# Performance work log

Measured on AMD Instinct MI355X. Metric: run time of the kernel, lower is better.

Reference implementation:

```python
import jax, jax.numpy as jnp
import numpy as np

B, T, VOCAB_SZ, N_SPK = 64, 1024, 34, 128
D_TXT, D_SPK, H, N_MELS = 512, 64, 256, 80


def _lstm_params(key, in_dim, hid):
    k1, k2, k3, k4 = jax.random.split(key, 4)
    s = 1.0 / np.sqrt(hid)
    Wih = jax.random.uniform(k1, (4 * hid, in_dim), jnp.float32, -s, s)
    Whh = jax.random.uniform(k2, (4 * hid, hid), jnp.float32, -s, s)
    bih = jax.random.uniform(k3, (4 * hid,), jnp.float32, -s, s)
    bhh = jax.random.uniform(k4, (4 * hid,), jnp.float32, -s, s)
    return Wih, Whh, bih, bhh


def setup_inputs() -> dict:
    key = jax.random.key(0)
    ks = jax.random.split(key, 10)
    text_seq = jax.random.randint(ks[0], (B, T), 0, VOCAB_SZ)
    mel_spectrogram = jax.random.normal(ks[1], (B, T, N_MELS), jnp.float32)
    speaker_id = jax.random.randint(ks[2], (B,), 0, N_SPK)
    emb_text = jax.random.normal(ks[3], (VOCAB_SZ, D_TXT), jnp.float32)
    emb_text = emb_text.at[0].set(0.0)  # padding_idx=0
    emb_spk = jax.random.normal(ks[4], (N_SPK, D_SPK), jnp.float32)
    Wih_f, Whh_f, bih_f, bhh_f = _lstm_params(ks[5], D_TXT + D_SPK, H)
    Wih_b, Whh_b, bih_b, bhh_b = _lstm_params(ks[6], D_TXT + D_SPK, H)
    Wih_d, _Whh_d, bih_d, bhh_d = _lstm_params(ks[7], N_MELS + 2 * H, H)
    s = 1.0 / np.sqrt(H)
    Wfc = jax.random.uniform(ks[8], (N_MELS, H), jnp.float32, -s, s)
    bfc = jax.random.uniform(ks[9], (N_MELS,), jnp.float32, -s, s)
    return dict(text_seq=text_seq, mel_spectrogram=mel_spectrogram, speaker_id=speaker_id,
                emb_text=emb_text, emb_spk=emb_spk,
                Wih_f=Wih_f, Whh_f=Whh_f, bih_f=bih_f, bhh_f=bhh_f,
                Wih_b=Wih_b, Whh_b=Whh_b, bih_b=bih_b, bhh_b=bhh_b,
                Wih_d=Wih_d, bih_d=bih_d, bhh_d=bhh_d, Wfc=Wfc, bfc=bfc)


def _lstm_scan(xs, Wih, Whh, bih, bhh, reverse=False):
    # xs: [T, B, D] -> hs: [T, B, H] (PyTorch gate order i,f,g,o)
    nB, hid = xs.shape[1], Whh.shape[1]
    bias = bih + bhh
    def step(carry, x):
        h, c = carry
        g = x @ Wih.T + h @ Whh.T + bias
        i, f, gg, o = jnp.split(g, 4, axis=-1)
        c = jax.nn.sigmoid(f) * c + jax.nn.sigmoid(i) * jnp.tanh(gg)
        h = jax.nn.sigmoid(o) * jnp.tanh(c)
        return (h, c), h
    init = (jnp.zeros((nB, hid), xs.dtype), jnp.zeros((nB, hid), xs.dtype))
    _, hs = jax.lax.scan(step, init, xs, reverse=reverse)
    return hs


def reference(text_seq, mel_spectrogram, speaker_id, emb_text, emb_spk,
              Wih_f, Whh_f, bih_f, bhh_f, Wih_b, Whh_b, bih_b, bhh_b,
              Wih_d, bih_d, bhh_d, Wfc, bfc):
    text_embed = emb_text[text_seq]                       # [B, T, 512]
    spk = jnp.broadcast_to(emb_spk[speaker_id][:, None, :],
                           (text_seq.shape[0], text_seq.shape[1], emb_spk.shape[1]))
    enc_in = jnp.concatenate([text_embed, spk], axis=-1)  # [B, T, 576]
    xs = jnp.transpose(enc_in, (1, 0, 2))                 # time-major [T, B, 576]
    h_fwd = _lstm_scan(xs, Wih_f, Whh_f, bih_f, bhh_f)
    h_bwd = _lstm_scan(xs, Wih_b, Whh_b, bih_b, bhh_b, reverse=True)
    enc_out = jnp.concatenate([h_fwd, h_bwd], axis=-1)    # [T, B, 512]

    max_len = min(mel_spectrogram.shape[1], enc_out.shape[0])
    # Decoder: hidden state is reset (None) every step in the original, so
    # c = sigmoid(i)*tanh(g), h = sigmoid(o)*tanh(c); Whh contributes nothing.
    dbias = bih_d + bhh_d
    def dstep(prev_mel, e_t):
        x = jnp.concatenate([prev_mel, e_t], axis=-1)     # [B, 592]
        g = x @ Wih_d.T + dbias
        i, f, gg, o = jnp.split(g, 4, axis=-1)
        c = jax.nn.sigmoid(i) * jnp.tanh(gg)
        h = jax.nn.sigmoid(o) * jnp.tanh(c)
        out = h @ Wfc.T + bfc
        return out, out
    _, outs = jax.lax.scan(dstep, mel_spectrogram[:, 0, :], enc_out[: max_len - 1])
    return jnp.transpose(outs, (1, 0, 2))                 # [B, max_len-1, 80]
```

## Files before the change

kernel.cpp:

```cpp
#include <hip/hip_runtime.h>
#include <hip/hip_fp16.h>
#include <stdint.h>

#define T_SEQ 1024
#define NB    64
#define VOCAB 34
#define NSPK  128
#define DTXT  512
#define HID   256
#define NMEL  80
#define GROWS 1024
#define DROWS 768

typedef _Float16 f16;
typedef _Float16 f16x2 __attribute__((ext_vector_type(2)));
typedef _Float16 v8h __attribute__((ext_vector_type(8)));
typedef float v4f __attribute__((ext_vector_type(4)));

__device__ __forceinline__ float fdot2f(uint32_t a, uint32_t b, float c) {
  return __builtin_amdgcn_fdot2(__builtin_bit_cast(f16x2, a),
                                __builtin_bit_cast(f16x2, b), c, false);
}
__device__ __forceinline__ float sigm(float x) { return 1.0f / (1.0f + __expf(-x)); }
__device__ __forceinline__ float tanhf_fast(float x) {
  float e = __expf(2.0f * x);
  return 1.0f - 2.0f / (e + 1.0f);
}


__global__ void k_tp(const float* __restrict__ Wf, const float* __restrict__ Wb,
                     const float* __restrict__ emb_text, float* __restrict__ TP) {
  int blk = blockIdx.x; int dir = blk / VOCAB; int v = blk - dir * VOCAB;
  const float* W = dir ? Wb : Wf;
  const float* e = emb_text + (size_t)v * DTXT;
  for (int r = threadIdx.x; r < GROWS; r += 256) {
    const float* wr = W + (size_t)r * 576;
    float a0 = 0, a1 = 0, a2 = 0, a3 = 0;
    for (int d = 0; d < DTXT; d += 4) {
      a0 += e[d] * wr[d];     a1 += e[d+1] * wr[d+1];
      a2 += e[d+2] * wr[d+2]; a3 += e[d+3] * wr[d+3];
    }
    TP[(size_t)(dir * VOCAB + v) * GROWS + r] = (a0 + a1) + (a2 + a3);
  }
}

__global__ void k_sp(const float* __restrict__ Wf, const float* __restrict__ Wb,
                     const float* __restrict__ bihf, const float* __restrict__ bhhf,
                     const float* __restrict__ bihb, const float* __restrict__ bhhb,
                     const float* __restrict__ emb_spk, float* __restrict__ SP) {
  int blk = blockIdx.x; int dir = blk >> 7; int s = blk & 127;
  const float* W  = dir ? Wb : Wf;
  const float* bi = dir ? bihb : bihf;
  const float* bh = dir ? bhhb : bhhf;
  const float* e  = emb_spk + (size_t)s * 64;
  for (int r = threadIdx.x; r < GROWS; r += 256) {
    const float* wr = W + (size_t)r * 576 + 512;
    float acc = bi[r] + bh[r];
    for (int d = 0; d < 64; ++d) acc += e[d] * wr[d];
    SP[(size_t)(dir * NSPK + s) * GROWS + r] = acc;
  }
}

__global__ void k_whh(const float* __restrict__ Whhf, const float* __restrict__ Whhb,
                      f16* __restrict__ WhhH) {
  int idx = blockIdx.x * 256 + threadIdx.x;
  if (idx < 2 * GROWS * HID) {
    int dir = idx >> 18; int rem = idx & (GROWS * HID - 1);
    WhhH[idx] = (f16)(dir ? Whhb[rem] : Whhf[rem]);
  }
}

__global__ void k_decw(const float* __restrict__ Wih_d, const float* __restrict__ bih_d,
                       const float* __restrict__ bhh_d,
                       f16* __restrict__ WmH, f16* __restrict__ WdH, float* __restrict__ dbias) {
  int r = blockIdx.x;
  int src = (r < 256) ? r : (r + 256);
  const float* w = Wih_d + (size_t)src * 592;
  for (int k = threadIdx.x; k < 592; k += 256) {
    float v = w[k];
    if (k < 80) WmH[(size_t)r * 80 + k] = (f16)v;
    else        WdH[(size_t)r * 512 + (k - 80)] = (f16)v;
  }
  if (threadIdx.x == 0) dbias[r] = bih_d[src] + bhh_d[src];
}

__global__ void k_misc(const float* __restrict__ Wfc, f16* __restrict__ WfcH) {
  int idx = blockIdx.x * 256 + threadIdx.x;
  if (idx < NMEL * HID) WfcH[idx] = (f16)Wfc[idx];
}

__launch_bounds__(512, 2)
__global__ void k_enc(const int* __restrict__ text_seq, const int* __restrict__ speaker_id,
                      const float* __restrict__ TP, const float* __restrict__ SP,
                      const uint32_t* __restrict__ WhhH_dw,
                      f16* __restrict__ Hh) {
  __shared__ __align__(16) uint4 wtail[8 * 512];
  __shared__ __align__(16) uint32_t hbuf[2][128];
  __shared__ float pp[4][256];
  __shared__ int tseq[T_SEQ];

  int wg = blockIdx.x;
  int dir = wg >> 6, b = wg & 63;
  int tid = threadIdx.x;
  int u = tid & 255, kh = tid >> 8;

  uint4 w0[14], w1[14], w2[14], w3[14];
  {
    const uint4* p0 = (const uint4*)(WhhH_dw + ((size_t)(dir << 10) + u      ) * 128 + (kh << 6));
    const uint4* p1 = (const uint4*)(WhhH_dw + ((size_t)(dir << 10) + u + 256) * 128 + (kh << 6));
    const uint4* p2 = (const uint4*)(WhhH_dw + ((size_t)(dir << 10) + u + 512) * 128 + (kh << 6));
    const uint4* p3 = (const uint4*)(WhhH_dw + ((size_t)(dir << 10) + u + 768) * 128 + (kh << 6));
    #pragma unroll
    for (int i = 0; i < 14; ++i) { w0[i] = p0[i]; w1[i] = p1[i]; w2[i] = p2[i]; w3[i] = p3[i]; }
    #pragma unroll
    for (int j = 0; j < 2; ++j) {
      wtail[(0 * 2 + j) * 512 + tid] = p0[14 + j];
      wtail[(1 * 2 + j) * 512 + tid] = p1[14 + j];
      wtail[(2 * 2 + j) * 512 + tid] = p2[14 + j];
      wtail[(3 * 2 + j) * 512 + tid] = p3[14 + j];
    }
  }
  for (int i = tid; i < T_SEQ; i += 512) tseq[i] = text_seq[b * T_SEQ + i];
  if (tid < 128) hbuf[0][tid] = 0u;
  float sp0 = 0, sp1 = 0, sp2 = 0, sp3 = 0;
  if (kh == 0) {
    int spk = speaker_id[b];
    sp0 = SP[(size_t)(dir * NSPK + spk) * GROWS + u];
    sp1 = SP[(size_t)(dir * NSPK + spk) * GROWS + u + 256];
    sp2 = SP[(size_t)(dir * NSPK + spk) * GROWS + u + 512];
    sp3 = SP[(size_t)(dir * NSPK + spk) * GROWS + u + 768];
  }
  const float* TPd = TP + (size_t)dir * VOCAB * GROWS;
  float c_state = 0.0f;
  __syncthreads();

  float x0 = 0, x1 = 0, x2 = 0, x3 = 0;
  if (kh == 0) {
    int v = tseq[dir ? (T_SEQ - 1) : 0];
    x0 = TPd[(size_t)v * GROWS + u];
    x1 = TPd[(size_t)v * GROWS + u + 256];
    x2 = TPd[(size_t)v * GROWS + u + 512];
    x3 = TPd[(size_t)v * GROWS + u + 768];
  }

  float h_keep = 0.0f; int t_keep = 0;
  for (int n = 0; n < T_SEQ; ++n) {
    int t = dir ? (T_SEQ - 1 - n) : n;
    float xn0 = 0, xn1 = 0, xn2 = 0, xn3 = 0;
    if (kh == 0) {
      if (n > 0)
        Hh[((size_t)(dir * T_SEQ + t_keep) * NB + b) * HID + u] = (f16)h_keep;
      int tn = dir ? (T_SEQ - 2 - n) : (n + 1);
      tn = tn < 0 ? 0 : (tn > T_SEQ - 1 ? T_SEQ - 1 : tn);
      int vn = tseq[tn];
      xn0 = TPd[(size_t)vn * GROWS + u];
      xn1 = TPd[(size_t)vn * GROWS + u + 256];
      xn2 = TPd[(size_t)vn * GROWS + u + 512];
      xn3 = TPd[(size_t)vn * GROWS + u + 768];
    }

    float i0 = 0, i1 = 0, f0 = 0, f1 = 0, g0 = 0, g1 = 0, o0 = 0, o1 = 0;
    const uint4* h4 = ((const uint4*)hbuf[n & 1]) + (kh << 4);
    #pragma unroll
    for (int c = 0; c < 14; ++c) {
      uint4 hv = h4[c];
      i0 = fdot2f(w0[c].x, hv.x, i0); f0 = fdot2f(w1[c].x, hv.x, f0);
      g0 = fdot2f(w2[c].x, hv.x, g0); o0 = fdot2f(w3[c].x, hv.x, o0);
      i1 = fdot2f(w0[c].y, hv.y, i1); f1 = fdot2f(w1[c].y, hv.y, f1);
      g1 = fdot2f(w2[c].y, hv.y, g1); o1 = fdot2f(w3[c].y, hv.y, o1);
      i0 = fdot2f(w0[c].z, hv.z, i0); f0 = fdot2f(w1[c].z, hv.z, f0);
      g0 = fdot2f(w2[c].z, hv.z, g0); o0 = fdot2f(w3[c].z, hv.z, o0);
      i1 = fdot2f(w0[c].w, hv.w, i1); f1 = fdot2f(w1[c].w, hv.w, f1);
      g1 = fdot2f(w2[c].w, hv.w, g1); o1 = fdot2f(w3[c].w, hv.w, o1);
    }
    #pragma unroll
    for (int j = 0; j < 2; ++j) {
      uint4 hv = h4[14 + j];
      uint4 t0v = wtail[(0 * 2 + j) * 512 + tid];
      uint4 t1v = wtail[(1 * 2 + j) * 512 + tid];
      uint4 t2v = wtail[(2 * 2 + j) * 512 + tid];
      uint4 t3v = wtail[(3 * 2 + j) * 512 + tid];
      i0 = fdot2f(t0v.x, hv.x, i0); f0 = fdot2f(t1v.x, hv.x, f0);
      g0 = fdot2f(t2v.x, hv.x, g0); o0 = fdot2f(t3v.x, hv.x, o0);
      i1 = fdot2f(t0v.y, hv.y, i1); f1 = fdot2f(t1v.y, hv.y, f1);
      g1 = fdot2f(t2v.y, hv.y, g1); o1 = fdot2f(t3v.y, hv.y, o1);
      i0 = fdot2f(t0v.z, hv.z, i0); f0 = fdot2f(t1v.z, hv.z, f0);
      g0 = fdot2f(t2v.z, hv.z, g0); o0 = fdot2f(t3v.z, hv.z, o0);
      i1 = fdot2f(t0v.w, hv.w, i1); f1 = fdot2f(t1v.w, hv.w, f1);
      g1 = fdot2f(t2v.w, hv.w, g1); o1 = fdot2f(t3v.w, hv.w, o1);
    }
    if (kh == 1) {
      pp[0][u] = i0 + i1;
      pp[1][u] = f0 + f1;
      pp[2][u] = g0 + g1;
      pp[3][u] = o0 + o1;
    }
    __syncthreads();

    if (kh == 0) {
      float gi = (i0 + i1) + pp[0][u] + x0 + sp0;
      float gf = (f0 + f1) + pp[1][u] + x1 + sp1;
      float gg = (g0 + g1) + pp[2][u] + x2 + sp2;
      float go = (o0 + o1) + pp[3][u] + x3 + sp3;
      c_state = sigm(gf) * c_state + sigm(gi) * tanhf_fast(gg);
      float h = sigm(go) * tanhf_fast(c_state);
      ((f16*)hbuf[(n + 1) & 1])[u] = (f16)h;
      h_keep = h; t_keep = t;
      x0 = xn0; x1 = xn1; x2 = xn2; x3 = xn3;
    }
    __syncthreads();
  }
  if (kh == 0)
    Hh[((size_t)(dir * T_SEQ + t_keep) * NB + b) * HID + u] = (f16)h_keep;
}

__launch_bounds__(256, 4)
__global__ void k_eproj(const uint32_t* __restrict__ Hdw, const uint32_t* __restrict__ WdH_dw,
                        const float* __restrict__ dbias, f16* __restrict__ E) {
  __shared__ __align__(16) uint32_t Asm[64][68];
  __shared__ __align__(16) uint32_t Wsm[64][68];
  int nt = blockIdx.x % 12;
  int t  = blockIdx.x / 12;
  int n0 = nt * 64;
  int tid = threadIdx.x;
  int wave = tid >> 6, lane = tid & 63;
  int lr = lane & 15, lg = lane >> 4;

  v4f acc0 = {0,0,0,0}, acc1 = {0,0,0,0}, acc2 = {0,0,0,0}, acc3 = {0,0,0,0};

  for (int ch = 0; ch < 4; ++ch) {
    int dirc = ch >> 1, koff = (ch & 1) * 64;
    {
      int bb = tid >> 2, p = tid & 3;
      const uint32_t* asrc = Hdw + ((size_t)(dirc * T_SEQ + t) * NB + bb) * 128 + koff + p * 4;
      const uint32_t* wsrc = WdH_dw + (size_t)(n0 + bb) * 256 + ch * 64 + p * 4;
      #pragma unroll
      for (int q = 0; q < 4; ++q) {
        *(uint4*)(&Asm[bb][p * 4 + q * 16]) = *(const uint4*)(asrc + q * 16);
        *(uint4*)(&Wsm[bb][p * 4 + q * 16]) = *(const uint4*)(wsrc + q * 16);
      }
    }
    __syncthreads();
    #pragma unroll
    for (int sub = 0; sub < 4; ++sub) {
      v8h af = __builtin_bit_cast(v8h, *(const uint4*)&Asm[wave * 16 + lr][sub * 16 + lg * 4]);
      v8h b0 = __builtin_bit_cast(v8h, *(const uint4*)&Wsm[ 0 + lr][sub * 16 + lg * 4]);
      v8h b1 = __builtin_bit_cast(v8h, *(const uint4*)&Wsm[16 + lr][sub * 16 + lg * 4]);
      v8h b2 = __builtin_bit_cast(v8h, *(const uint4*)&Wsm[32 + lr][sub * 16 + lg * 4]);
      v8h b3 = __builtin_bit_cast(v8h, *(const uint4*)&Wsm[48 + lr][sub * 16 + lg * 4]);
      acc0 = __builtin_amdgcn_mfma_f32_16x16x32_f16(af, b0, acc0, 0, 0, 0);
      acc1 = __builtin_amdgcn_mfma_f32_16x16x32_f16(af, b1, acc1, 0, 0, 0);
      acc2 = __builtin_amdgcn_mfma_f32_16x16x32_f16(af, b2, acc2, 0, 0, 0);
      acc3 = __builtin_amdgcn_mfma_f32_16x16x32_f16(af, b3, acc3, 0, 0, 0);
    }
    __syncthreads();
  }

  float db0 = dbias[n0 +  0 + lr];
  float db1 = dbias[n0 + 16 + lr];
  float db2 = dbias[n0 + 32 + lr];
  float db3 = dbias[n0 + 48 + lr];
  #pragma unroll
  for (int reg = 0; reg < 4; ++reg) {
    int m = wave * 16 + lg * 4 + reg;
    f16* Erow = E + ((size_t)t * NB + m) * DROWS + n0;
    Erow[ 0 + lr] = (f16)(acc0[reg] + db0);
    Erow[16 + lr] = (f16)(acc1[reg] + db1);
    Erow[32 + lr] = (f16)(acc2[reg] + db2);
    Erow[48 + lr] = (f16)(acc3[reg] + db3);
  }
}

__launch_bounds__(512, 2)
__global__ void k_dec(const float* __restrict__ mel, const f16* __restrict__ E,
                      const uint32_t* __restrict__ WmH_dw, const uint32_t* __restrict__ WfcH_dw,
                      const float* __restrict__ bfc, float* __restrict__ out) {
  __shared__ __align__(16) uint32_t pm[40];
  __shared__ __align__(16) uint32_t h_sm[128];
  __shared__ float pp[3][256];
  __shared__ float partial[80][4];
  __shared__ __align__(16) uint4 Ebuf[2][16 * 96];

  int b = blockIdx.x;
  int tid = threadIdx.x;
  int u = tid & 255, kh = tid >> 8;

  uint4 wm0[5], wm1[5], wm2[5];
  {
    const uint4* p0 = (const uint4*)(WmH_dw + (size_t)(u      ) * 40) + kh * 5;
    const uint4* p1 = (const uint4*)(WmH_dw + (size_t)(u + 256) * 40) + kh * 5;
    const uint4* p2 = (const uint4*)(WmH_dw + (size_t)(u + 512) * 40) + kh * 5;
    #pragma unroll
    for (int k = 0; k < 5; ++k) { wm0[k] = p0[k]; wm1[k] = p1[k]; wm2[k] = p2[k]; }
  }
  int fr = (tid < 320) ? (tid >> 2) : 0;
  int q  = tid & 3;
  uint4 wfc[8];
  {
    const uint4* wp = (const uint4*)(WfcH_dw + (size_t)fr * 128) + q * 8;
    #pragma unroll
    for (int k = 0; k < 8; ++k) wfc[k] = wp[k];
  }
  float bfcv = bfc[tid < NMEL ? tid : 0];
  if (tid < 40) {
    float m0 = mel[(size_t)b * T_SEQ * NMEL + 2 * tid];
    float m1 = mel[(size_t)b * T_SEQ * NMEL + 2 * tid + 1];
    f16x2 v; v[0] = (f16)m0; v[1] = (f16)m1;
    pm[tid] = __builtin_bit_cast(uint32_t, v);
  }

  int srow = tid >> 5, scol = tid & 31;
  {
    const uint4* src = (const uint4*)(E + ((size_t)srow * NB + b) * DROWS);
    Ebuf[0][srow * 96 + scol     ] = src[scol];
    Ebuf[0][srow * 96 + scol + 32] = src[scol + 32];
    Ebuf[0][srow * 96 + scol + 64] = src[scol + 64];
  }
  __syncthreads();

  float o_keep = 0.0f;
  for (int t = 0; t < T_SEQ - 1; ++t) {
    int w = t >> 4, s = t & 15;
    if (t > 0 && tid < NMEL)
      out[((size_t)b * (T_SEQ - 1) + (t - 1)) * NMEL + tid] = o_keep;
    uint4 st0, st1, st2;
    bool do_stage = (s == 0) && (w < 63);
    if (do_stage) {
      int rr = (w + 1) * 16 + srow; if (rr > T_SEQ - 2) rr = T_SEQ - 2;
      const uint4* src = (const uint4*)(E + ((size_t)rr * NB + b) * DROWS);
      st0 = src[scol]; st1 = src[scol + 32]; st2 = src[scol + 64];
    }

    float a0 = 0, a1 = 0, a2 = 0;
    const uint4* pm4 = ((const uint4*)pm) + kh * 5;
    #pragma unroll
    for (int k = 0; k < 5; ++k) {
      uint4 hp = pm4[k];
      a0 = fdot2f(wm0[k].x, hp.x, a0); a1 = fdot2f(wm1[k].x, hp.x, a1); a2 = fdot2f(wm2[k].x, hp.x, a2);
      a0 = fdot2f(wm0[k].y, hp.y, a0); a1 = fdot2f(wm1[k].y, hp.y, a1); a2 = fdot2f(wm2[k].y, hp.y, a2);
      a0 = fdot2f(wm0[k].z, hp.z, a0); a1 = fdot2f(wm1[k].z, hp.z, a1); a2 = fdot2f(wm2[k].z, hp.z, a2);
      a0 = fdot2f(wm0[k].w, hp.w, a0); a1 = fdot2f(wm1[k].w, hp.w, a1); a2 = fdot2f(wm2[k].w, hp.w, a2);
    }
    if (kh == 1) { pp[0][u] = a0; pp[1][u] = a1; pp[2][u] = a2; }
    __syncthreads();

    if (kh == 0) {
      const f16* Erow = (const f16*)&Ebuf[w & 1][s * 96];
      float gi = a0 + pp[0][u] + (float)Erow[u];
      float gg = a1 + pp[1][u] + (float)Erow[u + 256];
      float go = a2 + pp[2][u] + (float)Erow[u + 512];
      float cc = sigm(gi) * tanhf_fast(gg);
      float h  = sigm(go) * tanhf_fast(cc);
      ((f16*)h_sm)[u] = (f16)h;
    }
    if (do_stage) {
      Ebuf[(w + 1) & 1][srow * 96 + scol     ] = st0;
      Ebuf[(w + 1) & 1][srow * 96 + scol + 32] = st1;
      Ebuf[(w + 1) & 1][srow * 96 + scol + 64] = st2;
    }
    __syncthreads();

    if (tid < 320) {
      const uint4* hrow = ((const uint4*)h_sm) + q * 8;
      float s0 = 0, s1 = 0, s2 = 0, s3 = 0;
      #pragma unroll
      for (int kk = 0; kk < 8; ++kk) {
        uint4 hq = hrow[kk];
        s0 = fdot2f(wfc[kk].x, hq.x, s0); s1 = fdot2f(wfc[kk].y, hq.y, s1);
        s2 = fdot2f(wfc[kk].z, hq.z, s2); s3 = fdot2f(wfc[kk].w, hq.w, s3);
      }
      partial[fr][q] = (s0 + s1) + (s2 + s3);
    }
    __syncthreads();

    if (tid < NMEL) {
      float o = ((partial[tid][0] + partial[tid][1]) +
                 (partial[tid][2] + partial[tid][3])) + bfcv;
      o_keep = o;
      ((f16*)pm)[tid] = (f16)o;
    }
    __syncthreads();
  }
  if (tid < NMEL)
    out[((size_t)b * (T_SEQ - 1) + (T_SEQ - 2)) * NMEL + tid] = o_keep;
}

extern "C" void kernel_launch(void* const* d_in, const int* in_sizes, int n_in,
                              void* d_out, int out_size, void* d_ws, size_t ws_size,
                              hipStream_t stream) {
  const int*   text_seq   = (const int*)d_in[0];
  const float* mel        = (const float*)d_in[1];
  const int*   speaker_id = (const int*)d_in[2];
  const float* emb_text   = (const float*)d_in[3];
  const float* emb_spk    = (const float*)d_in[4];
  const float* Wih_f = (const float*)d_in[5];
  const float* Whh_f = (const float*)d_in[6];
  const float* bih_f = (const float*)d_in[7];
  const float* bhh_f = (const float*)d_in[8];
  const float* Wih_b = (const float*)d_in[9];
  const float* Whh_b = (const float*)d_in[10];
  const float* bih_b = (const float*)d_in[11];
  const float* bhh_b = (const float*)d_in[12];
  const float* Wih_d = (const float*)d_in[13];
  const float* bih_d = (const float*)d_in[14];
  const float* bhh_d = (const float*)d_in[15];
  const float* Wfc   = (const float*)d_in[16];
  const float* bfc   = (const float*)d_in[17];
  float* out = (float*)d_out;

  char* base = (char*)d_ws;
  size_t off = 0;
  auto take = [&](size_t n) -> char* {
    off = (off + 255) & ~(size_t)255;
    char* r = base + off;
    off += n;
    return r;
  };
  float*        TP    = (float*)take((size_t)2 * VOCAB * GROWS * 4);
  float*        SP    = (float*)take((size_t)2 * NSPK * GROWS * 4);
  f16*          WhhH  = (f16*)take((size_t)2 * GROWS * HID * 2);
  f16*          WmH   = (f16*)take((size_t)DROWS * 80 * 2);
  f16*          WdH   = (f16*)take((size_t)DROWS * 512 * 2);
  f16*          WfcH  = (f16*)take((size_t)NMEL * HID * 2);
  float*        dbias = (float*)take((size_t)DROWS * 4);
  f16*          Hh    = (f16*)take((size_t)2 * T_SEQ * NB * HID * 2);
  f16*          E     = (f16*)take((size_t)(T_SEQ - 1) * NB * DROWS * 2);
  if (off > ws_size) return;

  k_tp  <<<2 * VOCAB, 256, 0, stream>>>(Wih_f, Wih_b, emb_text, TP);
  k_sp  <<<2 * NSPK, 256, 0, stream>>>(Wih_f, Wih_b, bih_f, bhh_f, bih_b, bhh_b, emb_spk, SP);
  k_whh <<<2048, 256, 0, stream>>>(Whh_f, Whh_b, WhhH);
  k_decw<<<DROWS, 256, 0, stream>>>(Wih_d, bih_d, bhh_d, WmH, WdH, dbias);
  k_misc<<<80, 256, 0, stream>>>(Wfc, WfcH);
  k_enc <<<128, 512, 0, stream>>>(text_seq, speaker_id, TP, SP,
                                  (const uint32_t*)WhhH, Hh);
  k_eproj<<<(T_SEQ - 1) * 12, 256, 0, stream>>>((const uint32_t*)Hh,
                                                (const uint32_t*)WdH, dbias, E);
  k_dec <<<NB, 512, 0, stream>>>(mel, E, (const uint32_t*)WmH,
                                 (const uint32_t*)WfcH, bfc, out);
}
```

Measured before the change: 3.023 ms.

## Pair adjacent lanes for K-split and reduce via shuffles instead of LDS barriers

Remaps the encoder and decoder threads so the two K-halves of each hidden unit sit in adjacent lanes and combines them with a lane shuffle, removing the LDS partial-sum buffers and one block barrier per time step. The decoder's FC reduction likewise uses shuffles across four adjacent lanes, which drops another barrier per step. Both lanes of a pair now compute the gate nonlinearities redundantly, and the encoder moves more of its Whh weights from registers to LDS (12 register chunks instead of 14), which adds LDS traffic in every step.

```diff
diff --git a/kernel.cpp b/kernel.cpp
--- a/kernel.cpp
+++ b/kernel.cpp
@@ -94,48 +94,44 @@
                       const float* __restrict__ TP, const float* __restrict__ SP,
                       const uint32_t* __restrict__ WhhH_dw,
                       f16* __restrict__ Hh) {
-  __shared__ __align__(16) uint4 wtail[8 * 512];
+  __shared__ __align__(16) uint4 wtail[16 * 512];
   __shared__ __align__(16) uint32_t hbuf[2][128];
-  __shared__ float pp[4][256];
   __shared__ int tseq[T_SEQ];
 
   int wg = blockIdx.x;
   int dir = wg >> 6, b = wg & 63;
   int tid = threadIdx.x;
-  int u = tid & 255, kh = tid >> 8;
-
-  uint4 w0[14], w1[14], w2[14], w3[14];
+  int u = tid >> 1, kh = tid & 1;
+
+  uint4 w0[12], w1[12], w2[12], w3[12];
   {
     const uint4* p0 = (const uint4*)(WhhH_dw + ((size_t)(dir << 10) + u      ) * 128 + (kh << 6));
     const uint4* p1 = (const uint4*)(WhhH_dw + ((size_t)(dir << 10) + u + 256) * 128 + (kh << 6));
     const uint4* p2 = (const uint4*)(WhhH_dw + ((size_t)(dir << 10) + u + 512) * 128 + (kh << 6));
     const uint4* p3 = (const uint4*)(WhhH_dw + ((size_t)(dir << 10) + u + 768) * 128 + (kh << 6));
     #pragma unroll
-    for (int i = 0; i < 14; ++i) { w0[i] = p0[i]; w1[i] = p1[i]; w2[i] = p2[i]; w3[i] = p3[i]; }
-    #pragma unroll
-    for (int j = 0; j < 2; ++j) {
-      wtail[(0 * 2 + j) * 512 + tid] = p0[14 + j];
-      wtail[(1 * 2 + j) * 512 + tid] = p1[14 + j];
-      wtail[(2 * 2 + j) * 512 + tid] = p2[14 + j];
-      wtail[(3 * 2 + j) * 512 + tid] = p3[14 + j];
+    for (int i = 0; i < 12; ++i) { w0[i] = p0[i]; w1[i] = p1[i]; w2[i] = p2[i]; w3[i] = p3[i]; }
+    #pragma unroll
+    for (int j = 0; j < 4; ++j) {
+      wtail[(0 * 4 + j) * 512 + tid] = p0[12 + j];
+      wtail[(1 * 4 + j) * 512 + tid] = p1[12 + j];
+      wtail[(2 * 4 + j) * 512 + tid] = p2[12 + j];
+      wtail[(3 * 4 + j) * 512 + tid] = p3[12 + j];
     }
   }
   for (int i = tid; i < T_SEQ; i += 512) tseq[i] = text_seq[b * T_SEQ + i];
   if (tid < 128) hbuf[0][tid] = 0u;
-  float sp0 = 0, sp1 = 0, sp2 = 0, sp3 = 0;
-  if (kh == 0) {
-    int spk = speaker_id[b];
-    sp0 = SP[(size_t)(dir * NSPK + spk) * GROWS + u];
-    sp1 = SP[(size_t)(dir * NSPK + spk) * GROWS + u + 256];
-    sp2 = SP[(size_t)(dir * NSPK + spk) * GROWS + u + 512];
-    sp3 = SP[(size_t)(dir * NSPK + spk) * GROWS + u + 768];
-  }
+  int spk = speaker_id[b];
+  float sp0 = SP[(size_t)(dir * NSPK + spk) * GROWS + u];
+  float sp1 = SP[(size_t)(dir * NSPK + spk) * GROWS + u + 256];
+  float sp2 = SP[(size_t)(dir * NSPK + spk) * GROWS + u + 512];
+  float sp3 = SP[(size_t)(dir * NSPK + spk) * GROWS + u + 768];
   const float* TPd = TP + (size_t)dir * VOCAB * GROWS;
   float c_state = 0.0f;
   __syncthreads();
 
-  float x0 = 0, x1 = 0, x2 = 0, x3 = 0;
-  if (kh == 0) {
+  float x0, x1, x2, x3;
+  {
     int v = tseq[dir ? (T_SEQ - 1) : 0];
     x0 = TPd[(size_t)v * GROWS + u];
     x1 = TPd[(size_t)v * GROWS + u + 256];
@@ -146,23 +142,20 @@
   float h_keep = 0.0f; int t_keep = 0;
   for (int n = 0; n < T_SEQ; ++n) {
     int t = dir ? (T_SEQ - 1 - n) : n;
-    float xn0 = 0, xn1 = 0, xn2 = 0, xn3 = 0;
-    if (kh == 0) {
-      if (n > 0)
-        Hh[((size_t)(dir * T_SEQ + t_keep) * NB + b) * HID + u] = (f16)h_keep;
-      int tn = dir ? (T_SEQ - 2 - n) : (n + 1);
-      tn = tn < 0 ? 0 : (tn > T_SEQ - 1 ? T_SEQ - 1 : tn);
-      int vn = tseq[tn];
-      xn0 = TPd[(size_t)vn * GROWS + u];
-      xn1 = TPd[(size_t)vn * GROWS + u + 256];
-      xn2 = TPd[(size_t)vn * GROWS + u + 512];
-      xn3 = TPd[(size_t)vn * GROWS + u + 768];
-    }
+    if (kh == 1 && n > 0)
+      Hh[((size_t)(dir * T_SEQ + t_keep) * NB + b) * HID + u] = (f16)h_keep;
+    int tn = dir ? (T_SEQ - 2 - n) : (n + 1);
+    tn = tn < 0 ? 0 : (tn > T_SEQ - 1 ? T_SEQ - 1 : tn);
+    int vn = tseq[tn];
+    float xn0 = TPd[(size_t)vn * GROWS + u];
+    float xn1 = TPd[(size_t)vn * GROWS + u + 256];
+    float xn2 = TPd[(size_t)vn * GROWS + u + 512];
+    float xn3 = TPd[(size_t)vn * GROWS + u + 768];
 
     float i0 = 0, i1 = 0, f0 = 0, f1 = 0, g0 = 0, g1 = 0, o0 = 0, o1 = 0;
     const uint4* h4 = ((const uint4*)hbuf[n & 1]) + (kh << 4);
     #pragma unroll
-    for (int c = 0; c < 14; ++c) {
+    for (int c = 0; c < 12; ++c) {
       uint4 hv = h4[c];
       i0 = fdot2f(w0[c].x, hv.x, i0); f0 = fdot2f(w1[c].x, hv.x, f0);
       g0 = fdot2f(w2[c].x, hv.x, g0); o0 = fdot2f(w3[c].x, hv.x, o0);
@@ -174,12 +167,12 @@
       g1 = fdot2f(w2[c].w, hv.w, g1); o1 = fdot2f(w3[c].w, hv.w, o1);
     }
     #pragma unroll
-    for (int j = 0; j < 2; ++j) {
-      uint4 hv = h4[14 + j];
-      uint4 t0v = wtail[(0 * 2 + j) * 512 + tid];
-      uint4 t1v = wtail[(1 * 2 + j) * 512 + tid];
-      uint4 t2v = wtail[(2 * 2 + j) * 512 + tid];
-      uint4 t3v = wtail[(3 * 2 + j) * 512 + tid];
+    for (int j = 0; j < 4; ++j) {
+      uint4 hv = h4[12 + j];
+      uint4 t0v = wtail[(0 * 4 + j) * 512 + tid];
+      uint4 t1v = wtail[(1 * 4 + j) * 512 + tid];
+      uint4 t2v = wtail[(2 * 4 + j) * 512 + tid];
+      uint4 t3v = wtail[(3 * 4 + j) * 512 + tid];
       i0 = fdot2f(t0v.x, hv.x, i0); f0 = fdot2f(t1v.x, hv.x, f0);
       g0 = fdot2f(t2v.x, hv.x, g0); o0 = fdot2f(t3v.x, hv.x, o0);
       i1 = fdot2f(t0v.y, hv.y, i1); f1 = fdot2f(t1v.y, hv.y, f1);
@@ -189,28 +182,18 @@
       i1 = fdot2f(t0v.w, hv.w, i1); f1 = fdot2f(t1v.w, hv.w, f1);
       g1 = fdot2f(t2v.w, hv.w, g1); o1 = fdot2f(t3v.w, hv.w, o1);
     }
-    if (kh == 1) {
-      pp[0][u] = i0 + i1;
-      pp[1][u] = f0 + f1;
-      pp[2][u] = g0 + g1;
-      pp[3][u] = o0 + o1;
-    }
+    float gi = i0 + i1, gf = f0 + f1, gg = g0 + g1, go = o0 + o1;
+    gi += __shfl_xor(gi, 1); gf += __shfl_xor(gf, 1);
+    gg += __shfl_xor(gg, 1); go += __shfl_xor(go, 1);
+    gi += x0 + sp0; gf += x1 + sp1; gg += x2 + sp2; go += x3 + sp3;
+    c_state = sigm(gf) * c_state + sigm(gi) * tanhf_fast(gg);
+    float h = sigm(go) * tanhf_fast(c_state);
+    if (kh == 0) ((f16*)hbuf[(n + 1) & 1])[u] = (f16)h;
+    h_keep = h; t_keep = t;
+    x0 = xn0; x1 = xn1; x2 = xn2; x3 = xn3;
     __syncthreads();
-
-    if (kh == 0) {
-      float gi = (i0 + i1) + pp[0][u] + x0 + sp0;
-      float gf = (f0 + f1) + pp[1][u] + x1 + sp1;
-      float gg = (g0 + g1) + pp[2][u] + x2 + sp2;
-      float go = (o0 + o1) + pp[3][u] + x3 + sp3;
-      c_state = sigm(gf) * c_state + sigm(gi) * tanhf_fast(gg);
-      float h = sigm(go) * tanhf_fast(c_state);
-      ((f16*)hbuf[(n + 1) & 1])[u] = (f16)h;
-      h_keep = h; t_keep = t;
-      x0 = xn0; x1 = xn1; x2 = xn2; x3 = xn3;
-    }
-    __syncthreads();
-  }
-  if (kh == 0)
+  }
+  if (kh == 1)
     Hh[((size_t)(dir * T_SEQ + t_keep) * NB + b) * HID + u] = (f16)h_keep;
 }
 
@@ -277,13 +260,11 @@
                       const float* __restrict__ bfc, float* __restrict__ out) {
   __shared__ __align__(16) uint32_t pm[40];
   __shared__ __align__(16) uint32_t h_sm[128];
-  __shared__ float pp[3][256];
-  __shared__ float partial[80][4];
   __shared__ __align__(16) uint4 Ebuf[2][16 * 96];
 
   int b = blockIdx.x;
   int tid = threadIdx.x;
-  int u = tid & 255, kh = tid >> 8;
+  int u = tid >> 1, kh = tid & 1;
 
   uint4 wm0[5], wm1[5], wm2[5];
   {
@@ -301,7 +282,7 @@
     #pragma unroll
     for (int k = 0; k < 8; ++k) wfc[k] = wp[k];
   }
-  float bfcv = bfc[tid < NMEL ? tid : 0];
+  float bfcv = bfc[fr];
   if (tid < 40) {
     float m0 = mel[(size_t)b * T_SEQ * NMEL + 2 * tid];
     float m1 = mel[(size_t)b * T_SEQ * NMEL + 2 * tid + 1];
@@ -321,8 +302,8 @@
   float o_keep = 0.0f;
   for (int t = 0; t < T_SEQ - 1; ++t) {
     int w = t >> 4, s = t & 15;
-    if (t > 0 && tid < NMEL)
-      out[((size_t)b * (T_SEQ - 1) + (t - 1)) * NMEL + tid] = o_keep;
+    if (t > 0 && tid < 320 && q == 0)
+      out[((size_t)b * (T_SEQ - 1) + (t - 1)) * NMEL + fr] = o_keep;
     uint4 st0, st1, st2;
     bool do_stage = (s == 0) && (w < 63);
     if (do_stage) {
@@ -341,17 +322,15 @@
       a0 = fdot2f(wm0[k].z, hp.z, a0); a1 = fdot2f(wm1[k].z, hp.z, a1); a2 = fdot2f(wm2[k].z, hp.z, a2);
       a0 = fdot2f(wm0[k].w, hp.w, a0); a1 = fdot2f(wm1[k].w, hp.w, a1); a2 = fdot2f(wm2[k].w, hp.w, a2);
     }
-    if (kh == 1) { pp[0][u] = a0; pp[1][u] = a1; pp[2][u] = a2; }
-    __syncthreads();
-
-    if (kh == 0) {
+    a0 += __shfl_xor(a0, 1); a1 += __shfl_xor(a1, 1); a2 += __shfl_xor(a2, 1);
+    {
       const f16* Erow = (const f16*)&Ebuf[w & 1][s * 96];
-      float gi = a0 + pp[0][u] + (float)Erow[u];
-      float gg = a1 + pp[1][u] + (float)Erow[u + 256];
-      float go = a2 + pp[2][u] + (float)Erow[u + 512];
+      float gi = a0 + (float)Erow[u];
+      float gg = a1 + (float)Erow[u + 256];
+      float go = a2 + (float)Erow[u + 512];
       float cc = sigm(gi) * tanhf_fast(gg);
       float h  = sigm(go) * tanhf_fast(cc);
-      ((f16*)h_sm)[u] = (f16)h;
+      if (kh == 0) ((f16*)h_sm)[u] = (f16)h;
     }
     if (do_stage) {
       Ebuf[(w + 1) & 1][srow * 96 + scol     ] = st0;
@@ -369,20 +348,19 @@
         s0 = fdot2f(wfc[kk].x, hq.x, s0); s1 = fdot2f(wfc[kk].y, hq.y, s1);
         s2 = fdot2f(wfc[kk].z, hq.z, s2); s3 = fdot2f(wfc[kk].w, hq.w, s3);
       }
-      partial[fr][q] = (s0 + s1) + (s2 + s3);
+      float sv = (s0 + s1) + (s2 + s3);
+      sv += __shfl_xor(sv, 1);
+      sv += __shfl_xor(sv, 2);
+      if (q == 0) {
+        float o = sv + bfcv;
+        o_keep = o;
+        ((f16*)pm)[fr] = (f16)o;
+      }
     }
     __syncthreads();
-
-    if (tid < NMEL) {
-      float o = ((partial[tid][0] + partial[tid][1]) +
-                 (partial[tid][2] + partial[tid][3])) + bfcv;
-      o_keep = o;
-      ((f16*)pm)[tid] = (f16)o;
-    }
-    __syncthreads();
-  }
-  if (tid < NMEL)
-    out[((size_t)b * (T_SEQ - 1) + (T_SEQ - 2)) * NMEL + tid] = o_keep;
+  }
+  if (tid < 320 && q == 0)
+    out[((size_t)b * (T_SEQ - 1) + (T_SEQ - 2)) * NMEL + fr] = o_keep;
 }
 
 extern "C" void kernel_launch(void* const* d_in, const int* in_sizes, int n_in,
```

Result: no change. 3.000 ms (-0.7%).

## Fold Wfc into decoder input weights so recurrence runs directly on h

Applied to the files above, without the earlier changes.

Precomputes Wm·Wfc (a 768x256 matrix) and Wm·bfc on device, so each decoder step computes gates from the previous hidden state rather than waiting for the 80-wide mel output. The output projection is then computed off the critical path from the double-buffered h and written directly with shuffle reductions. This cuts per-step barriers from three to one and replaces the cross-half LDS partial sums with lane-pair shuffles. In exchange the recurrent dot product grows from 80 to 256 wide, and the prior output is no longer rounded to fp16 before feeding back, which changes numerics slightly. The encoder also moves more Whh columns from registers into LDS to relieve register pressure.

```diff
diff --git a/kernel.cpp b/kernel.cpp
--- a/kernel.cpp
+++ b/kernel.cpp
@@ -84,6 +84,23 @@
   if (threadIdx.x == 0) dbias[r] = bih_d[src] + bhh_d[src];
 }
 
+__global__ void k_wmf(const float* __restrict__ Wih_d, const float* __restrict__ Wfc,
+                      const float* __restrict__ bfc,
+                      f16* __restrict__ WmfH, float* __restrict__ mb) {
+  int r = blockIdx.x;
+  int src = (r < 256) ? r : (r + 256);
+  const float* wrow = Wih_d + (size_t)src * 592;
+  int k = threadIdx.x;
+  float acc = 0.0f;
+  for (int m = 0; m < NMEL; ++m) acc += wrow[m] * Wfc[(size_t)m * HID + k];
+  WmfH[(size_t)r * HID + k] = (f16)acc;
+  if (k == 0) {
+    float a = 0.0f;
+    for (int m = 0; m < NMEL; ++m) a += wrow[m] * bfc[m];
+    mb[r] = a;
+  }
+}
+
 __global__ void k_misc(const float* __restrict__ Wfc, f16* __restrict__ WfcH) {
   int idx = blockIdx.x * 256 + threadIdx.x;
   if (idx < NMEL * HID) WfcH[idx] = (f16)Wfc[idx];
@@ -94,7 +111,7 @@
                       const float* __restrict__ TP, const float* __restrict__ SP,
                       const uint32_t* __restrict__ WhhH_dw,
                       f16* __restrict__ Hh) {
-  __shared__ __align__(16) uint4 wtail[8 * 512];
+  __shared__ __align__(16) uint4 wtail[16 * 512];
   __shared__ __align__(16) uint32_t hbuf[2][128];
   __shared__ float pp[4][256];
   __shared__ int tseq[T_SEQ];
@@ -104,20 +121,20 @@
   int tid = threadIdx.x;
   int u = tid & 255, kh = tid >> 8;
 
-  uint4 w0[14], w1[14], w2[14], w3[14];
+  uint4 w0[12], w1[12], w2[12], w3[12];
   {
     const uint4* p0 = (const uint4*)(WhhH_dw + ((size_t)(dir << 10) + u      ) * 128 + (kh << 6));
     const uint4* p1 = (const uint4*)(WhhH_dw + ((size_t)(dir << 10) + u + 256) * 128 + (kh << 6));
     const uint4* p2 = (const uint4*)(WhhH_dw + ((size_t)(dir << 10) + u + 512) * 128 + (kh << 6));
     const uint4* p3 = (const uint4*)(WhhH_dw + ((size_t)(dir << 10) + u + 768) * 128 + (kh << 6));
     #pragma unroll
-    for (int i = 0; i < 14; ++i) { w0[i] = p0[i]; w1[i] = p1[i]; w2[i] = p2[i]; w3[i] = p3[i]; }
-    #pragma unroll
-    for (int j = 0; j < 2; ++j) {
-      wtail[(0 * 2 + j) * 512 + tid] = p0[14 + j];
-      wtail[(1 * 2 + j) * 512 + tid] = p1[14 + j];
-      wtail[(2 * 2 + j) * 512 + tid] = p2[14 + j];
-      wtail[(3 * 2 + j) * 512 + tid] = p3[14 + j];
+    for (int i = 0; i < 12; ++i) { w0[i] = p0[i]; w1[i] = p1[i]; w2[i] = p2[i]; w3[i] = p3[i]; }
+    #pragma unroll
+    for (int j = 0; j < 4; ++j) {
+      wtail[(0 * 4 + j) * 512 + tid] = p0[12 + j];
+      wtail[(1 * 4 + j) * 512 + tid] = p1[12 + j];
+      wtail[(2 * 4 + j) * 512 + tid] = p2[12 + j];
+      wtail[(3 * 4 + j) * 512 + tid] = p3[12 + j];
     }
   }
   for (int i = tid; i < T_SEQ; i += 512) tseq[i] = text_seq[b * T_SEQ + i];
@@ -162,7 +179,7 @@
     float i0 = 0, i1 = 0, f0 = 0, f1 = 0, g0 = 0, g1 = 0, o0 = 0, o1 = 0;
     const uint4* h4 = ((const uint4*)hbuf[n & 1]) + (kh << 4);
     #pragma unroll
-    for (int c = 0; c < 14; ++c) {
+    for (int c = 0; c < 12; ++c) {
       uint4 hv = h4[c];
       i0 = fdot2f(w0[c].x, hv.x, i0); f0 = fdot2f(w1[c].x, hv.x, f0);
       g0 = fdot2f(w2[c].x, hv.x, g0); o0 = fdot2f(w3[c].x, hv.x, o0);
@@ -174,12 +191,12 @@
       g1 = fdot2f(w2[c].w, hv.w, g1); o1 = fdot2f(w3[c].w, hv.w, o1);
     }
     #pragma unroll
-    for (int j = 0; j < 2; ++j) {
-      uint4 hv = h4[14 + j];
-      uint4 t0v = wtail[(0 * 2 + j) * 512 + tid];
-      uint4 t1v = wtail[(1 * 2 + j) * 512 + tid];
-      uint4 t2v = wtail[(2 * 2 + j) * 512 + tid];
-      uint4 t3v = wtail[(3 * 2 + j) * 512 + tid];
+    for (int j = 0; j < 4; ++j) {
+      uint4 hv = h4[12 + j];
+      uint4 t0v = wtail[(0 * 4 + j) * 512 + tid];
+      uint4 t1v = wtail[(1 * 4 + j) * 512 + tid];
+      uint4 t2v = wtail[(2 * 4 + j) * 512 + tid];
+      uint4 t3v = wtail[(3 * 4 + j) * 512 + tid];
       i0 = fdot2f(t0v.x, hv.x, i0); f0 = fdot2f(t1v.x, hv.x, f0);
       g0 = fdot2f(t2v.x, hv.x, g0); o0 = fdot2f(t3v.x, hv.x, o0);
       i1 = fdot2f(t0v.y, hv.y, i1); f1 = fdot2f(t1v.y, hv.y, f1);
@@ -273,26 +290,33 @@
 
 __launch_bounds__(512, 2)
 __global__ void k_dec(const float* __restrict__ mel, const f16* __restrict__ E,
-                      const uint32_t* __restrict__ WmH_dw, const uint32_t* __restrict__ WfcH_dw,
+                      const uint32_t* __restrict__ WmH_dw, const uint32_t* __restrict__ WmfH_dw,
+                      const uint32_t* __restrict__ WfcH_dw, const float* __restrict__ mb,
                       const float* __restrict__ bfc, float* __restrict__ out) {
-  __shared__ __align__(16) uint32_t pm[40];
-  __shared__ __align__(16) uint32_t h_sm[128];
-  __shared__ float pp[3][256];
-  __shared__ float partial[80][4];
+  __shared__ __align__(16) uint32_t pm0[40];
+  __shared__ __align__(16) uint32_t h_dbl[2][128];
+  __shared__ __align__(16) uint4 wtl[12 * 512];
   __shared__ __align__(16) uint4 Ebuf[2][16 * 96];
 
   int b = blockIdx.x;
   int tid = threadIdx.x;
-  int u = tid & 255, kh = tid >> 8;
-
-  uint4 wm0[5], wm1[5], wm2[5];
+  int u = tid >> 1, kh = tid & 1;
+
+  uint4 w0[12], w1[12], w2[12];
   {
-    const uint4* p0 = (const uint4*)(WmH_dw + (size_t)(u      ) * 40) + kh * 5;
-    const uint4* p1 = (const uint4*)(WmH_dw + (size_t)(u + 256) * 40) + kh * 5;
-    const uint4* p2 = (const uint4*)(WmH_dw + (size_t)(u + 512) * 40) + kh * 5;
-    #pragma unroll
-    for (int k = 0; k < 5; ++k) { wm0[k] = p0[k]; wm1[k] = p1[k]; wm2[k] = p2[k]; }
-  }
+    const uint4* p0 = (const uint4*)(WmfH_dw + (size_t)(u      ) * 128) + kh * 16;
+    const uint4* p1 = (const uint4*)(WmfH_dw + (size_t)(u + 256) * 128) + kh * 16;
+    const uint4* p2 = (const uint4*)(WmfH_dw + (size_t)(u + 512) * 128) + kh * 16;
+    #pragma unroll
+    for (int i = 0; i < 12; ++i) { w0[i] = p0[i]; w1[i] = p1[i]; w2[i] = p2[i]; }
+    #pragma unroll
+    for (int j = 0; j < 4; ++j) {
+      wtl[(0 * 4 + j) * 512 + tid] = p0[12 + j];
+      wtl[(1 * 4 + j) * 512 + tid] = p1[12 + j];
+      wtl[(2 * 4 + j) * 512 + tid] = p2[12 + j];
+    }
+  }
+  float mb0 = mb[u], mb1 = mb[u + 256], mb2 = mb[u + 512];
   int fr = (tid < 320) ? (tid >> 2) : 0;
   int q  = tid & 3;
   uint4 wfc[8];
@@ -301,12 +325,12 @@
     #pragma unroll
     for (int k = 0; k < 8; ++k) wfc[k] = wp[k];
   }
-  float bfcv = bfc[tid < NMEL ? tid : 0];
+  float bfcv = bfc[fr];
   if (tid < 40) {
     float m0 = mel[(size_t)b * T_SEQ * NMEL + 2 * tid];
     float m1 = mel[(size_t)b * T_SEQ * NMEL + 2 * tid + 1];
     f16x2 v; v[0] = (f16)m0; v[1] = (f16)m1;
-    pm[tid] = __builtin_bit_cast(uint32_t, v);
+    pm0[tid] = __builtin_bit_cast(uint32_t, v);
   }
 
   int srow = tid >> 5, scol = tid & 31;
@@ -318,71 +342,110 @@
   }
   __syncthreads();
 
-  float o_keep = 0.0f;
-  for (int t = 0; t < T_SEQ - 1; ++t) {
-    int w = t >> 4, s = t & 15;
-    if (t > 0 && tid < NMEL)
-      out[((size_t)b * (T_SEQ - 1) + (t - 1)) * NMEL + tid] = o_keep;
-    uint4 st0, st1, st2;
-    bool do_stage = (s == 0) && (w < 63);
-    if (do_stage) {
+  {
+    const uint4* q0 = (const uint4*)(WmH_dw + (size_t)(u      ) * 40) + kh * 5;
+    const uint4* q1 = (const uint4*)(WmH_dw + (size_t)(u + 256) * 40) + kh * 5;
+    const uint4* q2 = (const uint4*)(WmH_dw + (size_t)(u + 512) * 40) + kh * 5;
+    const uint4* pmp = ((const uint4*)pm0) + kh * 5;
+    float a0 = 0, a1 = 0, a2 = 0;
+    #pragma unroll
+    for (int k = 0; k < 5; ++k) {
+      uint4 hp = pmp[k]; uint4 v0 = q0[k], v1 = q1[k], v2 = q2[k];
+      a0 = fdot2f(v0.x, hp.x, a0); a1 = fdot2f(v1.x, hp.x, a1); a2 = fdot2f(v2.x, hp.x, a2);
+      a0 = fdot2f(v0.y, hp.y, a0); a1 = fdot2f(v1.y, hp.y, a1); a2 = fdot2f(v2.y, hp.y, a2);
+      a0 = fdot2f(v0.z, hp.z, a0); a1 = fdot2f(v1.z, hp.z, a1); a2 = fdot2f(v2.z, hp.z, a2);
+      a0 = fdot2f(v0.w, hp.w, a0); a1 = fdot2f(v1.w, hp.w, a1); a2 = fdot2f(v2.w, hp.w, a2);
+    }
+    a0 += __shfl_xor(a0, 1); a1 += __shfl_xor(a1, 1); a2 += __shfl_xor(a2, 1);
+    const f16* Er = (const f16*)&Ebuf[0][0];
+    float gi = a0 + (float)Er[u];
+    float gg = a1 + (float)Er[u + 256];
+    float go = a2 + (float)Er[u + 512];
+    float cc = sigm(gi) * tanhf_fast(gg);
+    float h  = sigm(go) * tanhf_fast(cc);
+    if (kh == 0) ((f16*)h_dbl[0])[u] = (f16)h;
+  }
+
+  uint4 st0, st1, st2; bool pend = false; int wpend = 0;
+  for (int t = 1; t < T_SEQ - 1; ++t) {
+    __syncthreads();
+    int w = t >> 4, s = t & 15, cur = (t - 1) & 1;
+    if (s == 1 && w < 63) {
       int rr = (w + 1) * 16 + srow; if (rr > T_SEQ - 2) rr = T_SEQ - 2;
       const uint4* src = (const uint4*)(E + ((size_t)rr * NB + b) * DROWS);
       st0 = src[scol]; st1 = src[scol + 32]; st2 = src[scol + 64];
+      pend = true; wpend = w + 1;
+    }
+    if (s == 8 && pend) {
+      Ebuf[wpend & 1][srow * 96 + scol     ] = st0;
+      Ebuf[wpend & 1][srow * 96 + scol + 32] = st1;
+      Ebuf[wpend & 1][srow * 96 + scol + 64] = st2;
+      pend = false;
     }
 
     float a0 = 0, a1 = 0, a2 = 0;
-    const uint4* pm4 = ((const uint4*)pm) + kh * 5;
-    #pragma unroll
-    for (int k = 0; k < 5; ++k) {
-      uint4 hp = pm4[k];
-      a0 = fdot2f(wm0[k].x, hp.x, a0); a1 = fdot2f(wm1[k].x, hp.x, a1); a2 = fdot2f(wm2[k].x, hp.x, a2);
-      a0 = fdot2f(wm0[k].y, hp.y, a0); a1 = fdot2f(wm1[k].y, hp.y, a1); a2 = fdot2f(wm2[k].y, hp.y, a2);
-      a0 = fdot2f(wm0[k].z, hp.z, a0); a1 = fdot2f(wm1[k].z, hp.z, a1); a2 = fdot2f(wm2[k].z, hp.z, a2);
-      a0 = fdot2f(wm0[k].w, hp.w, a0); a1 = fdot2f(wm1[k].w, hp.w, a1); a2 = fdot2f(wm2[k].w, hp.w, a2);
-    }
-    if (kh == 1) { pp[0][u] = a0; pp[1][u] = a1; pp[2][u] = a2; }
-    __syncthreads();
-
-    if (kh == 0) {
-      const f16* Erow = (const f16*)&Ebuf[w & 1][s * 96];
-      float gi = a0 + pp[0][u] + (float)Erow[u];
-      float gg = a1 + pp[1][u] + (float)Erow[u + 256];
-      float go = a2 + pp[2][u] + (float)Erow[u + 512];
+    const uint4* h4 = ((const uint4*)h_dbl[cur]) + kh * 16;
+    #pragma unroll
+    for (int c = 0; c < 12; ++c) {
+      uint4 hv = h4[c];
+      a0 = fdot2f(w0[c].x, hv.x, a0); a1 = fdot2f(w1[c].x, hv.x, a1); a2 = fdot2f(w2[c].x, hv.x, a2);
+      a0 = fdot2f(w0[c].y, hv.y, a0); a1 = fdot2f(w1[c].y, hv.y, a1); a2 = fdot2f(w2[c].y, hv.y, a2);
+      a0 = fdot2f(w0[c].z, hv.z, a0); a1 = fdot2f(w1[c].z, hv.z, a1); a2 = fdot2f(w2[c].z, hv.z, a2);
+      a0 = fdot2f(w0[c].w, hv.w, a0); a1 = fdot2f(w1[c].w, hv.w, a1); a2 = fdot2f(w2[c].w, hv.w, a2);
+    }
+    #pragma unroll
+    for (int j = 0; j < 4; ++j) {
+      uint4 hv = h4[12 + j];
+      uint4 t0v = wtl[(0 * 4 + j) * 512 + tid];
+      uint4 t1v = wtl[(1 * 4 + j) * 512 + tid];
+      uint4 t2v = wtl[(2 * 4 + j) * 512 + tid];
+      a0 = fdot2f(t0v.x, hv.x, a0); a1 = fdot2f(t1v.x, hv.x, a1); a2 = fdot2f(t2v.x, hv.x, a2);
+      a0 = fdot2f(t0v.y, hv.y, a0); a1 = fdot2f(t1v.y, hv.y, a1); a2 = fdot2f(t2v.y, hv.y, a2);
+      a0 = fdot2f(t0v.z, hv.z, a0); a1 = fdot2f(t1v.z, hv.z, a1); a2 = fdot2f(t2v.z, hv.z, a2);
+      a0 = fdot2f(t0v.w, hv.w, a0); a1 = fdot2f(t1v.w, hv.w, a1); a2 = fdot2f(t2v.w, hv.w, a2);
+    }
+    a0 += __shfl_xor(a0, 1); a1 += __shfl_xor(a1, 1); a2 += __shfl_xor(a2, 1);
+    {
+      const f16* Er = (const f16*)&Ebuf[w & 1][s * 96];
+      float gi = a0 + mb0 + (float)Er[u];
+      float gg = a1 + mb1 + (float)Er[u + 256];
+      float go = a2 + mb2 + (float)Er[u + 512];
       float cc = sigm(gi) * tanhf_fast(gg);
       float h  = sigm(go) * tanhf_fast(cc);
-      ((f16*)h_sm)[u] = (f16)h;
-    }
-    if (do_stage) {
-      Ebuf[(w + 1) & 1][srow * 96 + scol     ] = st0;
-      Ebuf[(w + 1) & 1][srow * 96 + scol + 32] = st1;
-      Ebuf[(w + 1) & 1][srow * 96 + scol + 64] = st2;
-    }
-    __syncthreads();
-
+      if (kh == 0) ((f16*)h_dbl[t & 1])[u] = (f16)h;
+    }
     if (tid < 320) {
-      const uint4* hrow = ((const uint4*)h_sm) + q * 8;
+      const uint4* hr = ((const uint4*)h_dbl[cur]) + q * 8;
       float s0 = 0, s1 = 0, s2 = 0, s3 = 0;
       #pragma unroll
       for (int kk = 0; kk < 8; ++kk) {
-        uint4 hq = hrow[kk];
+        uint4 hq = hr[kk];
         s0 = fdot2f(wfc[kk].x, hq.x, s0); s1 = fdot2f(wfc[kk].y, hq.y, s1);
         s2 = fdot2f(wfc[kk].z, hq.z, s2); s3 = fdot2f(wfc[kk].w, hq.w, s3);
       }
-      partial[fr][q] = (s0 + s1) + (s2 + s3);
-    }
-    __syncthreads();
-
-    if (tid < NMEL) {
-      float o = ((partial[tid][0] + partial[tid][1]) +
-                 (partial[tid][2] + partial[tid][3])) + bfcv;
-      o_keep = o;
-      ((f16*)pm)[tid] = (f16)o;
-    }
-    __syncthreads();
-  }
-  if (tid < NMEL)
-    out[((size_t)b * (T_SEQ - 1) + (T_SEQ - 2)) * NMEL + tid] = o_keep;
+      float sv = (s0 + s1) + (s2 + s3);
+      sv += __shfl_xor(sv, 1);
+      sv += __shfl_xor(sv, 2);
+      if (q == 0)
+        out[((size_t)b * (T_SEQ - 1) + (t - 1)) * NMEL + fr] = sv + bfcv;
+    }
+  }
+  __syncthreads();
+  if (tid < 320) {
+    const uint4* hr = ((const uint4*)h_dbl[(T_SEQ - 2) & 1]) + q * 8;
+    float s0 = 0, s1 = 0, s2 = 0, s3 = 0;
+    #pragma unroll
+    for (int kk = 0; kk < 8; ++kk) {
+      uint4 hq = hr[kk];
+      s0 = fdot2f(wfc[kk].x, hq.x, s0); s1 = fdot2f(wfc[kk].y, hq.y, s1);
+      s2 = fdot2f(wfc[kk].z, hq.z, s2); s3 = fdot2f(wfc[kk].w, hq.w, s3);
+    }
+    float sv = (s0 + s1) + (s2 + s3);
+    sv += __shfl_xor(sv, 1);
+    sv += __shfl_xor(sv, 2);
+    if (q == 0)
+      out[((size_t)b * (T_SEQ - 1) + (T_SEQ - 2)) * NMEL + fr] = sv + bfcv;
+  }
 }
 
 extern "C" void kernel_launch(void* const* d_in, const int* in_sizes, int n_in,
@@ -422,7 +485,9 @@
   f16*          WmH   = (f16*)take((size_t)DROWS * 80 * 2);
   f16*          WdH   = (f16*)take((size_t)DROWS * 512 * 2);
   f16*          WfcH  = (f16*)take((size_t)NMEL * HID * 2);
+  f16*          WmfH  = (f16*)take((size_t)DROWS * HID * 2);
   float*        dbias = (float*)take((size_t)DROWS * 4);
+  float*        mb    = (float*)take((size_t)DROWS * 4);
   f16*          Hh    = (f16*)take((size_t)2 * T_SEQ * NB * HID * 2);
   f16*          E     = (f16*)take((size_t)(T_SEQ - 1) * NB * DROWS * 2);
   if (off > ws_size) return;
@@ -431,11 +496,12 @@
   k_sp  <<<2 * NSPK, 256, 0, stream>>>(Wih_f, Wih_b, bih_f, bhh_f, bih_b, bhh_b, emb_spk, SP);
   k_whh <<<2048, 256, 0, stream>>>(Whh_f, Whh_b, WhhH);
   k_decw<<<DROWS, 256, 0, stream>>>(Wih_d, bih_d, bhh_d, WmH, WdH, dbias);
+  k_wmf <<<DROWS, 256, 0, stream>>>(Wih_d, Wfc, bfc, WmfH, mb);
   k_misc<<<80, 256, 0, stream>>>(Wfc, WfcH);
   k_enc <<<128, 512, 0, stream>>>(text_seq, speaker_id, TP, SP,
                                   (const uint32_t*)WhhH, Hh);
   k_eproj<<<(T_SEQ - 1) * 12, 256, 0, stream>>>((const uint32_t*)Hh,
                                                 (const uint32_t*)WdH, dbias, E);
-  k_dec <<<NB, 512, 0, stream>>>(mel, E, (const uint32_t*)WmH,
-                                 (const uint32_t*)WfcH, bfc, out);
-}
+  k_dec <<<NB, 512, 0, stream>>>(mel, E, (const uint32_t*)WmH, (const uint32_t*)WmfH,
+                                 (const uint32_t*)WfcH, mb, bfc, out);
+}
```

Result: slower. 3.533 ms (+16.9%).
